# Kernel optimization log

Measured on AMD Instinct MI355X. Metric: run time of the kernel, lower is better.

## Reference

```python
import jax, jax.numpy as jnp
import numpy as np

WS = 7          # window size
NUM_HEADS = 12

def _relative_position_index(ws):
    # Same construction as the torch module; pure numpy constants.
    coords = np.stack(np.meshgrid(np.arange(ws), np.arange(ws), indexing='ij'))  # [2, ws, ws]
    flat = coords.reshape(2, -1)                                                 # [2, N]
    rel = flat[:, :, None] - flat[:, None, :]                                    # [2, N, N]
    rel = rel.transpose(1, 2, 0).copy()                                          # [N, N, 2]
    rel[:, :, 0] += ws - 1
    rel[:, :, 1] += ws - 1
    rel[:, :, 0] *= 2 * ws - 1
    return rel.sum(-1)                                                           # [N, N] int

REL_IDX = jnp.asarray(_relative_position_index(WS))

def setup_inputs() -> dict:
    key = jax.random.key(0)
    ks = jax.random.split(key, 7)
    C, H = 384, NUM_HEADS
    B_, N = 2048, WS * WS
    return {
        "x": jax.random.normal(ks[0], (B_, N, C), jnp.float32),
        "mask": jax.random.normal(ks[1], (64, N, N), jnp.float32),
        "qkv_w": jax.random.normal(ks[2], (3 * C, C), jnp.float32) * 0.02,
        "qkv_b": jax.random.normal(ks[3], (3 * C,), jnp.float32) * 0.02,
        "proj_w": jax.random.normal(ks[4], (C, C), jnp.float32) * 0.02,
        "proj_b": jax.random.normal(ks[5], (C,), jnp.float32) * 0.02,
        "rpb_table": jax.random.normal(ks[6], ((2 * WS - 1) ** 2, H), jnp.float32) * 0.02,
    }

def reference(x, mask, qkv_w, qkv_b, proj_w, proj_b, rpb_table):
    B_, N, C = x.shape
    H = NUM_HEADS
    hd = C // H
    scale = hd ** (-0.5)

    qkv = x @ qkv_w.T + qkv_b                                   # [B_, N, 3C]
    qkv = qkv.reshape(B_, N, 3, H, hd).transpose(2, 0, 3, 1, 4)  # [3, B_, H, N, hd]
    q, k, v = qkv[0], qkv[1], qkv[2]

    attn = jnp.einsum('bhnd,bhmd->bhnm', q * scale, k)          # [B_, H, N, N]

    bias = rpb_table[REL_IDX]                                   # [N, N, H]
    attn = attn + bias.transpose(2, 0, 1)[None]                 # + [1, H, N, N]

    nw = mask.shape[0]
    attn = attn.reshape(B_ // nw, nw, H, N, N) + mask[None, :, None]
    attn = attn.reshape(B_, H, N, N)
    attn = jax.nn.softmax(attn, axis=-1)

    out = jnp.einsum('bhnm,bhmd->bhnd', attn, v)                # [B_, H, N, hd]
    out = out.transpose(0, 2, 1, 3).reshape(B_, N, C)
    return out @ proj_w.T + proj_b
```

## Files before the change

kernel.cpp:

```cpp
#include <hip/hip_runtime.h>
#include <stdint.h>
#include <stddef.h>

#define BWIN 2048
#define NTOK 49
#define CDIM 384
#define HNUM 12
#define HD   32
#define MTOT (BWIN * NTOK)
#define LOG2E 1.4426950408889634f
#define QSCALE ((float)(0.17677669529663687 * 1.4426950408889634))

typedef __attribute__((ext_vector_type(8))) short short8;
typedef __attribute__((ext_vector_type(4))) float floatx4;

__device__ __forceinline__ unsigned short f2bf(float f) {
    union { float f; unsigned u; } v; v.f = f;
    unsigned u = v.u;
    u = u + 0x7fffu + ((u >> 16) & 1u);
    return (unsigned short)(u >> 16);
}

__device__ __forceinline__ void gload16(const void* g, void* l) {
    __builtin_amdgcn_global_load_lds(
        (const __attribute__((address_space(1))) void*)g,
        (__attribute__((address_space(3))) void*)l, 16, 0, 0);
}

#define XBLK  18816
#define WQBLK 216
#define WPBLK 72
__global__ __launch_bounds__(256) void convert_kernel(
    const float* __restrict__ x, const float* __restrict__ wq,
    const float* __restrict__ wp, unsigned short* __restrict__ xbf,
    unsigned short* __restrict__ wqbf, unsigned short* __restrict__ wpbf)
{
    int bid = blockIdx.x;
    const float* src; unsigned short* dst; size_t base;
    if (bid < XBLK)              { src = x;  dst = xbf;  base = (size_t)bid * 2048; }
    else if (bid < XBLK + WQBLK) { src = wq; dst = wqbf; base = (size_t)(bid - XBLK) * 2048; }
    else                         { src = wp; dst = wpbf; base = (size_t)(bid - XBLK - WQBLK) * 2048; }
    const size_t i = base + (size_t)threadIdx.x * 8;
    float4 a = *(const float4*)(src + i);
    float4 b = *(const float4*)(src + i + 4);
    unsigned short o[8] = {f2bf(a.x), f2bf(a.y), f2bf(a.z), f2bf(a.w),
                           f2bf(b.x), f2bf(b.y), f2bf(b.z), f2bf(b.w)};
    *(uint4*)(dst + i) = *(uint4*)o;
}

__global__ __launch_bounds__(256) void bias_kernel(
    const float* __restrict__ mask, const float* __restrict__ rpb,
    float* __restrict__ cb)
{
    const int bm = blockIdx.x, h = blockIdx.y;
    const int tid = threadIdx.x;
    const int w = tid >> 6, lane = tid & 63;
    const int cg = lane & 15, rg = lane >> 4;
    const int rbase = 16 * w + (rg << 2);
    const float* mk = mask + (size_t)bm * (NTOK * NTOK);
    float o[16];
    #pragma unroll
    for (int j = 0; j < 4; ++j) {
        const int col = 16 * j + cg;
        const bool vc = col < NTOK;
        int yj = 0, xj = 0;
        if (vc) { yj = col / 7; xj = col - yj * 7; }
        #pragma unroll
        for (int r = 0; r < 4; ++r) {
            const int row = rbase + r;
            float v = -1e30f;
            if (vc && row < NTOK) {
                const int yi = row / 7, xi = row - yi * 7;
                const int rel = (yi - yj + 6) * 13 + (xi - xj + 6);
                v = (rpb[rel * HNUM + h] + mk[row * NTOK + col]) * LOG2E;
            }
            o[4 * j + r] = v;
        }
    }
    float* dst = cb + ((size_t)bm * HNUM + h) * 4096 + (size_t)tid * 16;
    #pragma unroll
    for (int j = 0; j < 4; ++j)
        *(float4*)(dst + 4 * j) = *(const float4*)(o + 4 * j);
}

__global__ __launch_bounds__(256) void qkv_kernel(
    const unsigned short* __restrict__ a, const unsigned short* __restrict__ b,
    const float* __restrict__ bias, unsigned short* __restrict__ outq)
{
    __shared__ __align__(16) unsigned short lA[128 * 32];
    __shared__ __align__(16) unsigned short lB[128 * 32];

    const int tid = threadIdx.x;
    const int lane = tid & 63, w = tid >> 6;
    const int tN = blockIdx.x * 128;
    const int tM = blockIdx.y * 128;

    const int srow = (w << 5) + (lane >> 2);
    const int scol = (lane & 3) << 3;
    const unsigned short* gA = a + (size_t)(tM + srow) * CDIM + scol;
    const unsigned short* gB = b + (size_t)(tN + srow) * CDIM + scol;
    unsigned short* lAb = lA + (w << 10);
    unsigned short* lBb = lB + (w << 10);

    const int wm = (w & 1) << 6, wn = (w >> 1) << 6;
    const int cg = lane & 15, rg = lane >> 4;

    floatx4 acc[4][4];
    #pragma unroll
    for (int i = 0; i < 4; ++i)
        #pragma unroll
        for (int j = 0; j < 4; ++j) acc[i][j] = (floatx4){0.f, 0.f, 0.f, 0.f};

    for (int k0 = 0; k0 < CDIM; k0 += 32) {
        __syncthreads();
        gload16(gA + k0,              lAb);
        gload16(gA + k0 + 16 * CDIM,  lAb + 512);
        gload16(gB + k0,              lBb);
        gload16(gB + k0 + 16 * CDIM,  lBb + 512);
        __syncthreads();

        short8 af[4], bfr[4];
        #pragma unroll
        for (int i = 0; i < 4; ++i)
            af[i] = *(const short8*)&lA[(wm + 16 * i + cg) * 32 + rg * 8];
        #pragma unroll
        for (int j = 0; j < 4; ++j)
            bfr[j] = *(const short8*)&lB[(wn + 16 * j + cg) * 32 + rg * 8];
        #pragma unroll
        for (int i = 0; i < 4; ++i)
            #pragma unroll
            for (int j = 0; j < 4; ++j)
                acc[i][j] = __builtin_amdgcn_mfma_f32_16x16x32_bf16(af[i], bfr[j], acc[i][j], 0, 0, 0);
    }

    const int r0 = tM + wm + (rg << 2);
    #pragma unroll
    for (int j = 0; j < 4; ++j) {
        const int col = tN + wn + 16 * j + cg;
        const float bv = bias[col];
        const int which = col / CDIM;
        const int rem = col - which * CDIM;
        const int h = rem >> 5, d = rem & 31;
        const float sc = (which == 0) ? QSCALE : 1.0f;
        #pragma unroll
        for (int i = 0; i < 4; ++i) {
            #pragma unroll
            for (int r = 0; r < 4; ++r) {
                const int row = r0 + 16 * i + r;
                const int bb = row / NTOK;
                const int n = row - bb * NTOK;
                const size_t oidx = ((((size_t)which * BWIN + bb) * HNUM + h) * NTOK + n) * HD + d;
                outq[oidx] = f2bf((acc[i][j][r] + bv) * sc);
            }
        }
    }
}

__global__ __launch_bounds__(256) void attn_kernel(
    const unsigned short* __restrict__ qkv, const float* __restrict__ cb,
    unsigned short* __restrict__ outa)
{
    __shared__ __align__(16) unsigned short lq[64][40];
    __shared__ __align__(16) unsigned short lk[64][40];
    __shared__ __align__(16) unsigned short lvt[32][72];
    __shared__ __align__(16) unsigned short lp[64][72];

    const int b = blockIdx.x, h = blockIdx.y;
    const int tid = threadIdx.x;
    const size_t WHICH = (size_t)BWIN * HNUM * NTOK * HD;
    const size_t base = ((size_t)b * HNUM + h) * (NTOK * HD);

    const float* cbp = cb + ((size_t)(b & 63) * HNUM + h) * 4096 + (size_t)tid * 16;
    floatx4 z[4];
    #pragma unroll
    for (int j = 0; j < 4; ++j) z[j] = *(const floatx4*)(cbp + 4 * j);

    for (int e = tid; e < 1152; e += 256)
        ((unsigned*)&lvt[0][0])[e] = 0u;
    if (tid < 240) {
        const int r = 49 + (tid >> 4), c = (tid & 15) * 2;
        *(unsigned*)&lq[r][c] = 0u;
        *(unsigned*)&lk[r][c] = 0u;
    }
    uint4 vreg;
    if (tid < 196) {
        const int n = tid >> 2, d = (tid & 3) * 8;
        *(uint4*)&lq[n][d] = *(const uint4*)(qkv + base + tid * 8);
        *(uint4*)&lk[n][d] = *(const uint4*)(qkv + base + WHICH + tid * 8);
        vreg = *(const uint4*)(qkv + base + 2 * WHICH + tid * 8);
    }
    __syncthreads();

    if (tid < 196) {
        const int n = tid >> 2, d0 = (tid & 3) * 8;
        const unsigned short* vp = (const unsigned short*)&vreg;
        #pragma unroll
        for (int jj = 0; jj < 8; ++jj)
            lvt[d0 + jj][n] = vp[jj];
    }

    const int w = tid >> 6, lane = tid & 63;
    const int cg = lane & 15;
    const int rg = lane >> 4;
    const int rbase = 16 * w + rg * 4;

    short8 aq = *(const short8*)&lq[16 * w + cg][rg * 8];
    floatx4 s[4];
    #pragma unroll
    for (int j = 0; j < 4; ++j) {
        short8 bk = *(const short8*)&lk[16 * j + cg][rg * 8];
        s[j] = __builtin_amdgcn_mfma_f32_16x16x32_bf16(aq, bk, z[j], 0, 0, 0);
    }

    float l[4] = {0.f, 0.f, 0.f, 0.f};
    #pragma unroll
    for (int j = 0; j < 4; ++j) {
        const int col = 16 * j + cg;
        #pragma unroll
        for (int r = 0; r < 4; ++r) {
            const float e = exp2f(s[j][r]);
            l[r] += e;
            lp[rbase + r][col] = f2bf(e);
        }
    }
    #pragma unroll
    for (int st = 1; st < 16; st <<= 1) {
        #pragma unroll
        for (int r = 0; r < 4; ++r) l[r] += __shfl_xor(l[r], st);
    }
    float linv[4];
    #pragma unroll
    for (int r = 0; r < 4; ++r) linv[r] = 1.f / l[r];
    __syncthreads();

    #pragma unroll
    for (int n = 0; n < 2; ++n) {
        floatx4 o = {0, 0, 0, 0};
        #pragma unroll
        for (int kk = 0; kk < 2; ++kk) {
            short8 ap = *(const short8*)&lp[16 * w + cg][kk * 32 + rg * 8];
            short8 bv = *(const short8*)&lvt[16 * n + cg][kk * 32 + rg * 8];
            o = __builtin_amdgcn_mfma_f32_16x16x32_bf16(ap, bv, o, 0, 0, 0);
        }
        #pragma unroll
        for (int r = 0; r < 4; ++r) {
            const int row = rbase + r;
            if (row < NTOK)
                outa[((size_t)b * NTOK + row) * CDIM + h * HD + n * 16 + cg] =
                    f2bf(o[r] * linv[r]);
        }
    }
}

__global__ __launch_bounds__(256) void proj_kernel(
    const unsigned short* __restrict__ a, const unsigned short* __restrict__ b,
    const float* __restrict__ bias, float* __restrict__ out)
{
    __shared__ __align__(16) unsigned short lA[128 * 32];
    __shared__ __align__(16) unsigned short lB[128 * 32];

    const int tid = threadIdx.x;
    const int lane = tid & 63, w = tid >> 6;
    const int tN = blockIdx.x * 128;
    const int tM = blockIdx.y * 128;

    const int srow = (w << 5) + (lane >> 2);
    const int scol = (lane & 3) << 3;
    const unsigned short* gA = a + (size_t)(tM + srow) * CDIM + scol;
    const unsigned short* gB = b + (size_t)(tN + srow) * CDIM + scol;
    unsigned short* lAb = lA + (w << 10);
    unsigned short* lBb = lB + (w << 10);

    const int wm = (w & 1) << 6, wn = (w >> 1) << 6;
    const int cg = lane & 15, rg = lane >> 4;

    floatx4 acc[4][4];
    #pragma unroll
    for (int i = 0; i < 4; ++i)
        #pragma unroll
        for (int j = 0; j < 4; ++j) acc[i][j] = (floatx4){0.f, 0.f, 0.f, 0.f};

    for (int k0 = 0; k0 < CDIM; k0 += 32) {
        __syncthreads();
        gload16(gA + k0,             lAb);
        gload16(gA + k0 + 16 * CDIM, lAb + 512);
        gload16(gB + k0,             lBb);
        gload16(gB + k0 + 16 * CDIM, lBb + 512);
        __syncthreads();

        short8 af[4], bfr[4];
        #pragma unroll
        for (int i = 0; i < 4; ++i)
            af[i] = *(const short8*)&lA[(wm + 16 * i + cg) * 32 + rg * 8];
        #pragma unroll
        for (int j = 0; j < 4; ++j)
            bfr[j] = *(const short8*)&lB[(wn + 16 * j + cg) * 32 + rg * 8];
        #pragma unroll
        for (int i = 0; i < 4; ++i)
            #pragma unroll
            for (int j = 0; j < 4; ++j)
                acc[i][j] = __builtin_amdgcn_mfma_f32_16x16x32_bf16(af[i], bfr[j], acc[i][j], 0, 0, 0);
    }

    const int r0 = tM + wm + (rg << 2);
    #pragma unroll
    for (int j = 0; j < 4; ++j) {
        const int col = tN + wn + 16 * j + cg;
        const float bv = bias[col];
        #pragma unroll
        for (int i = 0; i < 4; ++i) {
            #pragma unroll
            for (int r = 0; r < 4; ++r) {
                const int row = r0 + 16 * i + r;
                out[(size_t)row * CDIM + col] = acc[i][j][r] + bv;
            }
        }
    }
}

extern "C" void kernel_launch(void* const* d_in, const int* in_sizes, int n_in,
                              void* d_out, int out_size, void* d_ws, size_t ws_size,
                              hipStream_t stream) {
    const float* x      = (const float*)d_in[0];
    const float* mask   = (const float*)d_in[1];
    const float* qkv_w  = (const float*)d_in[2];
    const float* qkv_b  = (const float*)d_in[3];
    const float* proj_w = (const float*)d_in[4];
    const float* proj_b = (const float*)d_in[5];
    const float* rpb    = (const float*)d_in[6];
    float* out = (float*)d_out;

    unsigned short* ws_qkv  = (unsigned short*)d_ws;
    unsigned short* xbf     = ws_qkv + (size_t)3 * BWIN * HNUM * NTOK * HD;
    unsigned short* ws_attn = xbf;
    unsigned short* wqbf    = xbf + (size_t)MTOT * CDIM;
    unsigned short* wpbf    = wqbf + (size_t)3 * CDIM * CDIM;
    float* cbias            = (float*)(wpbf + (size_t)CDIM * CDIM);

    convert_kernel<<<XBLK + WQBLK + WPBLK, 256, 0, stream>>>(x, qkv_w, proj_w, xbf, wqbf, wpbf);
    bias_kernel<<<dim3(64, HNUM), 256, 0, stream>>>(mask, rpb, cbias);
    qkv_kernel<<<dim3(1152 / 128, MTOT / 128), 256, 0, stream>>>(xbf, wqbf, qkv_b, ws_qkv);
    attn_kernel<<<dim3(BWIN, HNUM), 256, 0, stream>>>(ws_qkv, cbias, ws_attn);
    proj_kernel<<<dim3(CDIM / 128, MTOT / 128), 256, 0, stream>>>(ws_attn, wpbf, proj_b, out);
}
```

Baseline: 624.2 us.

## Swizzle GEMM LDS layout, remap blocks across XCDs, reorder QKV epilogue stores

Both GEMM kernels now XOR-swizzle the LDS tile layout so the 16-byte fragment reads for MFMA avoid bank conflicts. They also switch to a 1D grid with a block-id remap that assigns contiguous tile ranges to each of the 8 XCDs for better L2 locality. The QKV epilogue precomputes per-column offsets and makes the column loop innermost to cut index arithmetic. The remap hardcodes the grid sizes (7056 and 2352 blocks), which must divide evenly by 8.

```diff
diff --git a/kernel.cpp b/kernel.cpp
--- a/kernel.cpp
+++ b/kernel.cpp
@@ -92,11 +92,15 @@
 
     const int tid = threadIdx.x;
     const int lane = tid & 63, w = tid >> 6;
-    const int tN = blockIdx.x * 128;
-    const int tM = blockIdx.y * 128;
-
-    const int srow = (w << 5) + (lane >> 2);
-    const int scol = (lane & 3) << 3;
+
+    const int bid = blockIdx.x;
+    const int wg = (bid & 7) * 882 + (bid >> 3);
+    const int tN = (wg % 9) * 128;
+    const int tM = (wg / 9) * 128;
+
+    const int X = (lane << 4) ^ (((lane >> 3) & 7) << 4);
+    const int srow = (w << 5) + (X >> 6);
+    const int scol = (X & 63) >> 1;
     const unsigned short* gA = a + (size_t)(tM + srow) * CDIM + scol;
     const unsigned short* gB = b + (size_t)(tN + srow) * CDIM + scol;
     unsigned short* lAb = lA + (w << 10);
@@ -110,6 +114,17 @@
     for (int i = 0; i < 4; ++i)
         #pragma unroll
         for (int j = 0; j < 4; ++j) acc[i][j] = (floatx4){0.f, 0.f, 0.f, 0.f};
+
+    int offA[4], offB[4];
+    #pragma unroll
+    for (int i = 0; i < 4; ++i) {
+        const int rowA = wm + 16 * i + cg;
+        const int sA = (rowA << 6) + (rg << 4);
+        offA[i] = sA ^ (((sA >> 7) & 7) << 4);
+        const int rowB = wn + 16 * i + cg;
+        const int sB = (rowB << 6) + (rg << 4);
+        offB[i] = sB ^ (((sB >> 7) & 7) << 4);
+    }
 
     for (int k0 = 0; k0 < CDIM; k0 += 32) {
         __syncthreads();
@@ -122,10 +137,10 @@
         short8 af[4], bfr[4];
         #pragma unroll
         for (int i = 0; i < 4; ++i)
-            af[i] = *(const short8*)&lA[(wm + 16 * i + cg) * 32 + rg * 8];
+            af[i] = *(const short8*)((const char*)lA + offA[i]);
         #pragma unroll
         for (int j = 0; j < 4; ++j)
-            bfr[j] = *(const short8*)&lB[(wn + 16 * j + cg) * 32 + rg * 8];
+            bfr[j] = *(const short8*)((const char*)lB + offB[j]);
         #pragma unroll
         for (int i = 0; i < 4; ++i)
             #pragma unroll
@@ -134,24 +149,30 @@
     }
 
     const int r0 = tM + wm + (rg << 2);
+    float bv[4], sc[4];
+    size_t cjo[4];
     #pragma unroll
     for (int j = 0; j < 4; ++j) {
         const int col = tN + wn + 16 * j + cg;
-        const float bv = bias[col];
+        bv[j] = bias[col];
         const int which = col / CDIM;
         const int rem = col - which * CDIM;
         const int h = rem >> 5, d = rem & 31;
-        const float sc = (which == 0) ? QSCALE : 1.0f;
-        #pragma unroll
-        for (int i = 0; i < 4; ++i) {
+        sc[j] = (which == 0) ? QSCALE : 1.0f;
+        cjo[j] = (size_t)which * (BWIN * HNUM * NTOK * HD)
+               + (size_t)h * (NTOK * HD) + d;
+    }
+    #pragma unroll
+    for (int i = 0; i < 4; ++i) {
+        #pragma unroll
+        for (int r = 0; r < 4; ++r) {
+            const int row = r0 + 16 * i + r;
+            const int bb = row / NTOK;
+            const int n = row - bb * NTOK;
+            const size_t ro = (size_t)bb * (HNUM * NTOK * HD) + (size_t)n * HD;
             #pragma unroll
-            for (int r = 0; r < 4; ++r) {
-                const int row = r0 + 16 * i + r;
-                const int bb = row / NTOK;
-                const int n = row - bb * NTOK;
-                const size_t oidx = ((((size_t)which * BWIN + bb) * HNUM + h) * NTOK + n) * HD + d;
-                outq[oidx] = f2bf((acc[i][j][r] + bv) * sc);
-            }
+            for (int j = 0; j < 4; ++j)
+                outq[cjo[j] + ro] = f2bf((acc[i][j][r] + bv[j]) * sc[j]);
         }
     }
 }
@@ -261,11 +282,15 @@
 
     const int tid = threadIdx.x;
     const int lane = tid & 63, w = tid >> 6;
-    const int tN = blockIdx.x * 128;
-    const int tM = blockIdx.y * 128;
-
-    const int srow = (w << 5) + (lane >> 2);
-    const int scol = (lane & 3) << 3;
+
+    const int bid = blockIdx.x;
+    const int wg = (bid & 7) * 294 + (bid >> 3);
+    const int tN = (wg % 3) * 128;
+    const int tM = (wg / 3) * 128;
+
+    const int X = (lane << 4) ^ (((lane >> 3) & 7) << 4);
+    const int srow = (w << 5) + (X >> 6);
+    const int scol = (X & 63) >> 1;
     const unsigned short* gA = a + (size_t)(tM + srow) * CDIM + scol;
     const unsigned short* gB = b + (size_t)(tN + srow) * CDIM + scol;
     unsigned short* lAb = lA + (w << 10);
@@ -279,6 +304,17 @@
     for (int i = 0; i < 4; ++i)
         #pragma unroll
         for (int j = 0; j < 4; ++j) acc[i][j] = (floatx4){0.f, 0.f, 0.f, 0.f};
+
+    int offA[4], offB[4];
+    #pragma unroll
+    for (int i = 0; i < 4; ++i) {
+        const int rowA = wm + 16 * i + cg;
+        const int sA = (rowA << 6) + (rg << 4);
+        offA[i] = sA ^ (((sA >> 7) & 7) << 4);
+        const int rowB = wn + 16 * i + cg;
+        const int sB = (rowB << 6) + (rg << 4);
+        offB[i] = sB ^ (((sB >> 7) & 7) << 4);
+    }
 
     for (int k0 = 0; k0 < CDIM; k0 += 32) {
         __syncthreads();
@@ -291,10 +327,10 @@
         short8 af[4], bfr[4];
         #pragma unroll
         for (int i = 0; i < 4; ++i)
-            af[i] = *(const short8*)&lA[(wm + 16 * i + cg) * 32 + rg * 8];
+            af[i] = *(const short8*)((const char*)lA + offA[i]);
         #pragma unroll
         for (int j = 0; j < 4; ++j)
-            bfr[j] = *(const short8*)&lB[(wn + 16 * j + cg) * 32 + rg * 8];
+            bfr[j] = *(const short8*)((const char*)lB + offB[j]);
         #pragma unroll
         for (int i = 0; i < 4; ++i)
             #pragma unroll
@@ -339,7 +375,7 @@
 
     convert_kernel<<<XBLK + WQBLK + WPBLK, 256, 0, stream>>>(x, qkv_w, proj_w, xbf, wqbf, wpbf);
     bias_kernel<<<dim3(64, HNUM), 256, 0, stream>>>(mask, rpb, cbias);
-    qkv_kernel<<<dim3(1152 / 128, MTOT / 128), 256, 0, stream>>>(xbf, wqbf, qkv_b, ws_qkv);
+    qkv_kernel<<<7056, 256, 0, stream>>>(xbf, wqbf, qkv_b, ws_qkv);
     attn_kernel<<<dim3(BWIN, HNUM), 256, 0, stream>>>(ws_qkv, cbias, ws_attn);
-    proj_kernel<<<dim3(CDIM / 128, MTOT / 128), 256, 0, stream>>>(ws_attn, wpbf, proj_b, out);
-}
+    proj_kernel<<<2352, 256, 0, stream>>>(ws_attn, wpbf, proj_b, out);
+}
```

Result: faster. 582.9 us (-6.6%).
